# Optimization experiments

Hardware: AMD Instinct MI355X
Metric: run time of the kernel (lower is better)

Reference implementation:

```python
import jax, jax.numpy as jnp
import numpy as np

K = 5            # srn kernel size (kernels[0])
EPSILON = 1e-3   # epsilons -> SRN additive noise scale
BN_EPS = 1e-5
NUM_SLICES = 3
OUT_CH = 64
CLASSES = 5


def _unfold(x, k):
    # torch.nn.Unfold, padding=0: (B, C*k*k, L), channel-major then (kh, kw) row-major
    B, C, H, W = x.shape
    Ho, Wo = H - k + 1, W - k + 1
    cols = jnp.stack([x[:, :, i:i + Ho, j:j + Wo]
                      for i in range(k) for j in range(k)], axis=2)  # (B,C,k*k,Ho,Wo)
    return cols.reshape(B, C * k * k, Ho * Wo), Ho, Wo


def _bn(x, g, b):
    # BatchNorm2d in training mode: batch statistics, biased variance
    m = x.mean((0, 2, 3), keepdims=True)
    v = x.var((0, 2, 3), keepdims=True)
    return (x - m) * jax.lax.rsqrt(v + BN_EPS) * g[None, :, None, None] + b[None, :, None, None]


def _conv(x, w, b):
    y = jax.lax.conv_general_dilated(x, w, (1, 1), 'VALID',
                                     dimension_numbers=('NCHW', 'OIHW', 'NCHW'))
    return y + b[None, :, None, None]


def _avgpool(x, s):
    B, C, H, W = x.shape
    return x.reshape(B, C, H // s, s, W // s, s).mean((3, 5))


def _maxpool(x, s):
    B, C, H, W = x.shape
    return x.reshape(B, C, H // s, s, W // s, s).max((3, 5))


def _srn(x, srn_w):
    B = x.shape[0]
    y, Ho, Wo = _unfold(x, K)                               # (B, n, L)
    y = y + EPSILON * jax.random.normal(jax.random.key(42), y.shape, y.dtype)
    gg = jnp.std(y, axis=1, ddof=1, keepdims=True)          # torch.std is unbiased
    y = y / gg
    O, C, _, _, S = srn_w.shape
    n = C * K * K
    X = srn_w.reshape(O, n, S)
    X = jnp.concatenate([jnp.ones((O, n, 1), X.dtype), X], axis=2)   # (O, n, S+1)
    Xcov = jnp.einsum('onf,ong->ofg', X, X)                 # X^T X, (O, 4, 4)
    Xinv = jnp.linalg.inv(Xcov)
    M = jnp.einsum('ofg,ong->ofn', Xinv, X)
    Wc = jnp.einsum('ofn,bnl->bofl', M, y)
    pred = jnp.einsum('onf,bofl->bonl', X, Wc)              # fitted values (B,O,n,L)
    err = jnp.mean((y[:, None] - pred) ** 2, axis=2)        # (B,O,L)
    err = err.reshape(B, O, Ho, Wo)
    A = (jnp.exp(-err) - np.exp(-1.0)) / (1.0 - np.exp(-1.0))
    return A - 0.5


def setup_inputs() -> dict:
    key = jax.random.key(0)
    ks = jax.random.split(key, 12)
    x = jax.random.normal(ks[0], (4, 3, 64, 64), jnp.float32)
    # xavier-style init scaled up for numerical stability of the small-matrix inverse
    srn_w = 0.05 * jax.random.normal(ks[1], (OUT_CH, 3, K, K, NUM_SLICES), jnp.float32)
    conv2_w = 0.05 * jax.random.normal(ks[2], (128, 64, 3, 3), jnp.float32)
    conv2_b = 0.01 * jax.random.normal(ks[3], (128,), jnp.float32)
    conv3_w = 0.05 * jax.random.normal(ks[4], (128, 128, 3, 3), jnp.float32)
    conv3_b = 0.01 * jax.random.normal(ks[5], (128,), jnp.float32)
    conv4_w = 0.05 * jax.random.normal(ks[6], (128, 128, 3, 3), jnp.float32)
    conv4_b = 0.01 * jax.random.normal(ks[7], (128,), jnp.float32)
    bn1_g = jnp.ones((64,), jnp.float32); bn1_b = jnp.zeros((64,), jnp.float32)
    bn2_g = jnp.ones((128,), jnp.float32); bn2_b = jnp.zeros((128,), jnp.float32)
    bn3_g = jnp.ones((128,), jnp.float32); bn3_b = jnp.zeros((128,), jnp.float32)
    bn4_g = jnp.ones((128,), jnp.float32); bn4_b = jnp.zeros((128,), jnp.float32)
    fc2_w = 0.05 * jax.random.normal(ks[8], (CLASSES, 128, 1, 1), jnp.float32)
    fc2_b = 0.01 * jax.random.normal(ks[9], (CLASSES,), jnp.float32)
    return dict(x=x, srn_w=srn_w, conv2_w=conv2_w, conv2_b=conv2_b,
                conv3_w=conv3_w, conv3_b=conv3_b, conv4_w=conv4_w, conv4_b=conv4_b,
                bn1_g=bn1_g, bn1_b=bn1_b, bn2_g=bn2_g, bn2_b=bn2_b,
                bn3_g=bn3_g, bn3_b=bn3_b, bn4_g=bn4_g, bn4_b=bn4_b,
                fc2_w=fc2_w, fc2_b=fc2_b)


def reference(x, srn_w, conv2_w, conv2_b, conv3_w, conv3_b, conv4_w, conv4_b,
              bn1_g, bn1_b, bn2_g, bn2_b, bn3_g, bn3_b, bn4_g, bn4_b,
              fc2_w, fc2_b):
    h = _srn(x, srn_w)                                      # (B,64,60,60)
    h = _avgpool(h, 2)
    h = _bn(h, bn1_g, bn1_b)
    h = jax.nn.relu(_bn(_conv(h, conv2_w, conv2_b), bn2_g, bn2_b))
    h = _avgpool(h, 2)
    h = jax.nn.relu(_bn(_conv(h, conv3_w, conv3_b), bn3_g, bn3_b))
    h = _maxpool(h, 2)
    h = jax.nn.relu(_bn(_conv(h, conv4_w, conv4_b), bn4_g, bn4_b))
    h = _maxpool(h, 4)                                      # (B,128,1,1)
    flat = h.reshape(h.shape[0], -1)                        # (B,128)
    return flat @ fc2_w.reshape(CLASSES, -1).T + fc2_b      # 1x1 conv == matmul
```

## Files before the change

kernel.cpp:

```cpp
#include <hip/hip_runtime.h>
#include <math.h>

__device__ __align__(16) float g_w2p[9 * 2304 * 4];
__device__ __align__(16) float g_w3p[17 * 2304 * 4];
__device__ __align__(16) float g_w4p[8 * 4608 * 4];
__device__ __align__(16) float g_h1[4 * 30 * 30 * 64];
__device__ __align__(16) float g_h2[4 * 14 * 14 * 4 * 128];
__device__ __align__(16) float g_h3[4 * 6 * 6 * 4 * 128];
__device__ __align__(16) float g_h4[4 * 16 * 128];

__global__ __launch_bounds__(256) void k_srn(const float* __restrict__ x,
                                             const float* __restrict__ srn_w,
                                             const float* __restrict__ w2,
                                             float* __restrict__ stats) {
    __shared__ __align__(16) float wlds[64 * 244];
    __shared__ float xsm[648];
    __shared__ float part[2 * 15 * 66];
    __shared__ float redS[256], redQ[256];
    int bid = blockIdx.x, t = threadIdx.x;
    int b = bid / 60, rem = bid % 60, r = rem >> 1, ch = rem & 1;

    for (int j = bid * 256 + t; j < 73728; j += 240 * 256) {
        int c = j & 3, s4 = j >> 2;
        int sl = s4 % 36, tmp = s4 / 36, oc_l = tmp & 63, blk = tmp >> 6;
        int it = blk & 3, ocg = blk >> 2;
        int kw = sl % 3, icq = (sl / 3) & 3, kh = sl / 12;
        int ic = it * 16 + icq * 4 + c;
        g_w2p[j] = w2[((ocg * 64 + oc_l) * 64 + ic) * 9 + kh * 3 + kw];
    }

    float4 wr[15];
#pragma unroll
    for (int k = 0; k < 15; k++) {
        int i4 = k * 256 + t;
        if (i4 < 3600) wr[k] = ((const float4*)srn_w)[i4];
    }
    float xr[3];
#pragma unroll
    for (int k = 0; k < 3; k++) {
        int i = t + k * 256;
        if (i < 648) {
            int c = i / 216, rm = i % 216, rr = rm / 36, col = rm % 36;
            int gc = ch * 30 + col; if (gc > 63) gc = 63;
            xr[k] = x[((b * 3 + c) * 64 + (2 * r + rr)) * 64 + gc];
        }
    }
#pragma unroll
    for (int k = 0; k < 15; k++) {
        int i4 = k * 256 + t;
        if (i4 < 3600) {
            float v[4] = { wr[k].x, wr[k].y, wr[k].z, wr[k].w };
#pragma unroll
            for (int e = 0; e < 4; e++) {
                int i = i4 * 4 + e, o = i / 225, j = i % 225;
                wlds[o * 244 + (j / 15) * 16 + (j % 15)] = v[e];
            }
        }
    }
#pragma unroll
    for (int k = 0; k < 3; k++) { int i = t + k * 256; if (i < 648) xsm[i] = xr[k]; }
    __syncthreads();

    int w = t >> 6, o = t & 63;
    int rw = w & 1, cq = w >> 1, base = cq * 16;

    float z1[16], z2[16], z3[16], s[16], q[16];
#pragma unroll
    for (int i = 0; i < 16; i++) { z1[i]=0; z2[i]=0; z3[i]=0; s[i]=0; q[i]=0; }

    for (int c = 0; c < 3; c++) {
#pragma unroll
        for (int kh = 0; kh < 5; kh++) {
            float xv[20];
#pragma unroll
            for (int k = 0; k < 20; k++) xv[k] = xsm[(c * 6 + rw + kh) * 36 + base + k];
            float wf[16];
            const float* wp = &wlds[o * 244 + (c * 5 + kh) * 16];
            *(float4*)&wf[0]  = *(const float4*)&wp[0];
            *(float4*)&wf[4]  = *(const float4*)&wp[4];
            *(float4*)&wf[8]  = *(const float4*)&wp[8];
            *(float4*)&wf[12] = *(const float4*)&wp[12];
#pragma unroll
            for (int kw = 0; kw < 5; kw++) {
                float w1 = wf[kw * 3], w2v = wf[kw * 3 + 1], w3v = wf[kw * 3 + 2];
#pragma unroll
                for (int i = 0; i < 16; i++) {
                    float v = xv[kw + i];
                    s[i] += v; q[i] += v * v;
                    z1[i] += w1 * v; z2[i] += w2v * v; z3[i] += w3v * v;
                }
            }
        }
    }

    float gm[16];
    {
        float c01=0,c02=0,c03=0,c11=0,c12=0,c13=0,c22=0,c23=0,c33=0;
#pragma unroll
        for (int row = 0; row < 15; row++) {
            float wf[16];
            const float* wp = &wlds[o * 244 + row * 16];
            *(float4*)&wf[0]  = *(const float4*)&wp[0];
            *(float4*)&wf[4]  = *(const float4*)&wp[4];
            *(float4*)&wf[8]  = *(const float4*)&wp[8];
            *(float4*)&wf[12] = *(const float4*)&wp[12];
#pragma unroll
            for (int kw = 0; kw < 5; kw++) {
                float w1 = wf[kw*3], w2v = wf[kw*3+1], w3v = wf[kw*3+2];
                c01 += w1; c02 += w2v; c03 += w3v;
                c11 += w1*w1; c12 += w1*w2v; c13 += w1*w3v;
                c22 += w2v*w2v; c23 += w2v*w3v; c33 += w3v*w3v;
            }
        }
        float A[4][8];
        A[0][0]=75.f; A[0][1]=c01; A[0][2]=c02; A[0][3]=c03;
        A[1][0]=c01;  A[1][1]=c11; A[1][2]=c12; A[1][3]=c13;
        A[2][0]=c02;  A[2][1]=c12; A[2][2]=c22; A[2][3]=c23;
        A[3][0]=c03;  A[3][1]=c13; A[3][2]=c23; A[3][3]=c33;
#pragma unroll
        for (int i = 0; i < 4; i++)
#pragma unroll
            for (int j = 0; j < 4; j++) A[i][4 + j] = (i == j) ? 1.f : 0.f;
#pragma unroll
        for (int p = 0; p < 4; p++) {
            float ip = 1.f / A[p][p];
#pragma unroll
            for (int j = 0; j < 8; j++) A[p][j] *= ip;
#pragma unroll
            for (int i = 0; i < 4; i++) if (i != p) {
                float f = A[i][p];
#pragma unroll
                for (int j = 0; j < 8; j++) A[i][j] -= f * A[p][j];
            }
        }
#pragma unroll
        for (int i = 0; i < 4; i++)
#pragma unroll
            for (int j = 0; j < 4; j++) gm[i * 4 + j] = A[i][4 + j];
    }

    const float C1 = 0.36787944117144233f;
    const float INV = 1.5819767068693265f;
#pragma unroll
    for (int pp = 0; pp < 8; pp++) {
        int pl = cq * 8 + pp;
        if (pl < 15) {
            float aa = 0.f;
#pragma unroll
            for (int e = 0; e < 2; e++) {
                int i = 2 * pp + e;
                float sum = s[i], sq = q[i];
                float gg2 = (sq - sum * sum * (1.f / 75.f)) * (1.f / 74.f);
                float zf[4] = { sum, z1[i], z2[i], z3[i] };
                float qf = 0.f;
#pragma unroll
                for (int f = 0; f < 4; f++) {
                    float acc = 0.f;
#pragma unroll
                    for (int h = 0; h < 4; h++) acc += gm[f * 4 + h] * zf[h];
                    qf += acc * zf[f];
                }
                float err = (sq - qf) / (75.f * gg2);
                aa += (expf(-err) - C1) * INV - 0.5f;
            }
            part[(rw * 15 + pl) * 66 + o] = 0.25f * aa;
        }
    }
    __syncthreads();

    int j = t >> 6;
    float ps = 0.f, pq = 0.f;
    for (int pl = j; pl < 15; pl += 4) {
        float v = part[pl * 66 + o] + part[(15 + pl) * 66 + o];
        g_h1[((b * 30 + r) * 30 + ch * 15 + pl) * 64 + o] = v;
        ps += v; pq += v * v;
    }
    redS[t] = ps; redQ[t] = pq;
    __syncthreads();
    if (t < 64) {
        atomicAdd(&stats[t],      redS[t] + redS[64 + t] + redS[128 + t] + redS[192 + t]);
        atomicAdd(&stats[64 + t], redQ[t] + redQ[64 + t] + redQ[128 + t] + redQ[192 + t]);
    }
}

__global__ __launch_bounds__(256) void k_conv2(const float* __restrict__ w3,
                                               const float* __restrict__ g1,
                                               const float* __restrict__ b1,
                                               float* __restrict__ stats) {
    __shared__ __align__(16) float ws[64 * 148];
    __shared__ __align__(16) float xs[3 * 30 * 64];
    __shared__ float redS[256], redQ[256];
    int blk = blockIdx.x;
    int b = blk / 56, rem = blk % 56, oh = rem >> 1, ocg = rem & 1;
    int t = threadIdx.x;
    int oc_l = t & 63, qtr = t >> 6, owb = qtr * 7;

    for (int j = blk * 256 + t; j < 147456; j += 224 * 256) {
        int c = j & 3, s4 = j >> 2;
        int sl = s4 % 36, tmp = s4 / 36, oc2 = tmp & 63, bk = tmp >> 6;
        int it = bk & 7, og = bk >> 3;
        int kw = sl % 3, icq = (sl / 3) & 3, kh = sl / 12;
        int ic = it * 16 + icq * 4 + c;
        g_w3p[j] = w3[((og * 64 + oc2) * 128 + ic) * 9 + kh * 3 + kw];
    }

    {
        int icb = (t & 15) * 4;
        float4 S = *(const float4*)&stats[icb], Q = *(const float4*)&stats[64 + icb];
        float4 G4 = *(const float4*)&g1[icb], B4 = *(const float4*)&b1[icb];
        float scv[4], shv[4];
        float mm[4] = { S.x, S.y, S.z, S.w }, qq[4] = { Q.x, Q.y, Q.z, Q.w };
        float gg[4] = { G4.x, G4.y, G4.z, G4.w }, bb[4] = { B4.x, B4.y, B4.z, B4.w };
#pragma unroll
        for (int c = 0; c < 4; c++) {
            float m = mm[c] * (1.f / 3600.f);
            float v = qq[c] * (1.f / 3600.f) - m * m;
            scv[c] = gg[c] * rsqrtf(v + 1e-5f);
            shv[c] = bb[c] - m * scv[c];
        }
        const float4* src4 = (const float4*)(g_h1 + (b * 900 + oh * 30) * 64);
        float4 xr[6];
#pragma unroll
        for (int k = 0; k < 6; k++) { int i4 = t + k * 256; if (i4 < 1440) xr[k] = src4[i4]; }
        const float4* wsrc0 = (const float4*)g_w2p;
        float4 wreg[9];
#pragma unroll
        for (int k = 0; k < 9; k++) wreg[k] = wsrc0[(ocg * 4) * 2304 + k * 256 + t];
#pragma unroll
        for (int k = 0; k < 6; k++) {
            int i4 = t + k * 256;
            if (i4 < 1440) {
                float4 v;
                v.x = xr[k].x * scv[0] + shv[0]; v.y = xr[k].y * scv[1] + shv[1];
                v.z = xr[k].z * scv[2] + shv[2]; v.w = xr[k].w * scv[3] + shv[3];
                *(float4*)&xs[i4 * 4] = v;
            }
        }
#pragma unroll
        for (int k = 0; k < 9; k++) {
            int idx = k * 256 + t;
            *(float4*)&ws[(idx / 36) * 148 + (idx % 36) * 4] = wreg[k];
        }
    }
    __syncthreads();

    float acc[7] = {0, 0, 0, 0, 0, 0, 0};
    const float4* wsrc = (const float4*)g_w2p + (ocg * 4) * 2304;
    for (int it = 0; it < 4; ++it) {
        float4 wreg[9];
        if (it < 3) {
#pragma unroll
            for (int k = 0; k < 9; k++) wreg[k] = wsrc[(it + 1) * 2304 + k * 256 + t];
        }
#pragma unroll 1
        for (int icq = 0; icq < 4; icq++) {
            int xoff = it * 16 + icq * 4;
#pragma unroll
            for (int kh = 0; kh < 3; kh++) {
                const float* wb = &ws[oc_l * 148 + (kh * 4 + icq) * 12];
                float4 w0 = *(const float4*)&wb[0];
                float4 w1 = *(const float4*)&wb[4];
                float4 w2v = *(const float4*)&wb[8];
                const float* xrow = &xs[(kh * 30 + owb) * 64 + xoff];
                float4 x0 = *(const float4*)&xrow[0];
                float4 x1 = *(const float4*)&xrow[64];
#pragma unroll
                for (int i = 0; i < 7; i++) {
                    float4 x2 = *(const float4*)&xrow[(i + 2) * 64];
                    acc[i] += w0.x * x0.x + w0.y * x0.y + w0.z * x0.z + w0.w * x0.w
                            + w1.x * x1.x + w1.y * x1.y + w1.z * x1.z + w1.w * x1.w
                            + w2v.x * x2.x + w2v.y * x2.y + w2v.z * x2.z + w2v.w * x2.w;
                    x0 = x1; x1 = x2;
                }
            }
        }
        if (it < 3) {
            __syncthreads();
#pragma unroll
            for (int k = 0; k < 9; k++) {
                int idx = k * 256 + t;
                *(float4*)&ws[(idx / 36) * 148 + (idx % 36) * 4] = wreg[k];
            }
            __syncthreads();
        }
    }
    int oc = ocg * 64 + oc_l;
    float ps = 0.f, pq = 0.f;
#pragma unroll
    for (int i = 0; i < 7; i++) {
        int ow = owb + i;
        g_h2[(((b * 14 + (oh >> 1)) * 14 + (ow >> 1)) * 4 + (oh & 1) * 2 + (ow & 1)) * 128 + oc] = acc[i];
        ps += acc[i]; pq += acc[i] * acc[i];
    }
    redS[t] = ps; redQ[t] = pq;
    __syncthreads();
    if (t < 64) {
        atomicAdd(&stats[128 + ocg * 64 + t], redS[t] + redS[64 + t] + redS[128 + t] + redS[192 + t]);
        atomicAdd(&stats[256 + ocg * 64 + t], redQ[t] + redQ[64 + t] + redQ[128 + t] + redQ[192 + t]);
    }
}

__global__ __launch_bounds__(256) void k_conv3(const float* __restrict__ w4,
                                               const float* __restrict__ g2,
                                               const float* __restrict__ b2,
                                               float* __restrict__ stats) {
    __shared__ __align__(16) float ws[64 * 148];
    __shared__ __align__(16) float xs[3 * 14 * 128];
    __shared__ float redS[256], redQ[256];
    int blk = blockIdx.x;
    int b = blk / 24, rem = blk % 24, oh = rem >> 1, ocg = rem & 1;
    int t = threadIdx.x;
    int oc_l = t & 63, qtr = t >> 6, owb = qtr * 3;

    for (int j = blk * 256 + t; j < 147456; j += 96 * 256) {
        int c = j & 3, s4 = j >> 2;
        int sl = s4 % 72, tmp = s4 / 72, oc2 = tmp & 15, blkq = tmp >> 4;
        int icq = blkq & 3, og = blkq >> 2;
        int kw = sl % 3, icb2 = (sl / 3) & 7, kh = sl / 24;
        int ic = icq * 32 + icb2 * 4 + c;
        g_w4p[j] = w4[((og * 16 + oc2) * 128 + ic) * 9 + kh * 3 + kw];
    }

    {
        int icb = (t & 31) * 4;
        float4 S = *(const float4*)&stats[128 + icb], Q = *(const float4*)&stats[256 + icb];
        float4 G4 = *(const float4*)&g2[icb], B4 = *(const float4*)&b2[icb];
        float scv[4], shv[4];
        float mm[4] = { S.x, S.y, S.z, S.w }, qq[4] = { Q.x, Q.y, Q.z, Q.w };
        float gg[4] = { G4.x, G4.y, G4.z, G4.w }, bb[4] = { B4.x, B4.y, B4.z, B4.w };
#pragma unroll
        for (int c = 0; c < 4; c++) {
            float m = mm[c] * (1.f / 3136.f);
            float v = qq[c] * (1.f / 3136.f) - m * m;
            scv[c] = gg[c] * rsqrtf(v + 1e-5f);
            shv[c] = bb[c] - m * scv[c];
        }
        const float4* wsrc0 = (const float4*)g_w3p;
        float4 wreg[9];
#pragma unroll
        for (int k = 0; k < 9; k++) wreg[k] = wsrc0[(ocg * 8) * 2304 + k * 256 + t];
        float4 pa[6], pb[6], pc[6], pd[6];
#pragma unroll
        for (int k = 0; k < 6; k++) {
            int i4 = t + k * 256;
            if (i4 < 1344) {
                int px = (i4 >> 5) % 14, rr = i4 / 448;
                const float4* p0 = (const float4*)&g_h2[(((b * 14 + oh + rr) * 14 + px) * 4) * 128 + (i4 & 31) * 4];
                pa[k] = p0[0]; pb[k] = p0[32]; pc[k] = p0[64]; pd[k] = p0[96];
            }
        }
#pragma unroll
        for (int k = 0; k < 9; k++) {
            int idx = k * 256 + t;
            *(float4*)&ws[(idx / 36) * 148 + (idx % 36) * 4] = wreg[k];
        }
#pragma unroll
        for (int k = 0; k < 6; k++) {
            int i4 = t + k * 256;
            if (i4 < 1344) {
                float4 o4;
                o4.x = 0.25f * (fmaxf(pa[k].x * scv[0] + shv[0], 0.f) + fmaxf(pb[k].x * scv[0] + shv[0], 0.f)
                              + fmaxf(pc[k].x * scv[0] + shv[0], 0.f) + fmaxf(pd[k].x * scv[0] + shv[0], 0.f));
                o4.y = 0.25f * (fmaxf(pa[k].y * scv[1] + shv[1], 0.f) + fmaxf(pb[k].y * scv[1] + shv[1], 0.f)
                              + fmaxf(pc[k].y * scv[1] + shv[1], 0.f) + fmaxf(pd[k].y * scv[1] + shv[1], 0.f));
                o4.z = 0.25f * (fmaxf(pa[k].z * scv[2] + shv[2], 0.f) + fmaxf(pb[k].z * scv[2] + shv[2], 0.f)
                              + fmaxf(pc[k].z * scv[2] + shv[2], 0.f) + fmaxf(pd[k].z * scv[2] + shv[2], 0.f));
                o4.w = 0.25f * (fmaxf(pa[k].w * scv[3] + shv[3], 0.f) + fmaxf(pb[k].w * scv[3] + shv[3], 0.f)
                              + fmaxf(pc[k].w * scv[3] + shv[3], 0.f) + fmaxf(pd[k].w * scv[3] + shv[3], 0.f));
                *(float4*)&xs[i4 * 4] = o4;
            }
        }
    }
    __syncthreads();

    float acc[3] = {0, 0, 0};
    const float4* wsrc = (const float4*)g_w3p + (ocg * 8) * 2304;
    for (int it = 0; it < 8; ++it) {
        float4 wreg[9];
        if (it < 7) {
#pragma unroll
            for (int k = 0; k < 9; k++) wreg[k] = wsrc[(it + 1) * 2304 + k * 256 + t];
        }
#pragma unroll 1
        for (int icq = 0; icq < 4; icq++) {
            int xoff = it * 16 + icq * 4;
#pragma unroll
            for (int kh = 0; kh < 3; kh++) {
                const float* wb = &ws[oc_l * 148 + (kh * 4 + icq) * 12];
                float4 w0 = *(const float4*)&wb[0];
                float4 w1 = *(const float4*)&wb[4];
                float4 w2v = *(const float4*)&wb[8];
                const float* xrow = &xs[(kh * 14 + owb) * 128 + xoff];
                float4 x0 = *(const float4*)&xrow[0];
                float4 x1 = *(const float4*)&xrow[128];
#pragma unroll
                for (int i = 0; i < 3; i++) {
                    float4 x2 = *(const float4*)&xrow[(i + 2) * 128];
                    acc[i] += w0.x * x0.x + w0.y * x0.y + w0.z * x0.z + w0.w * x0.w
                            + w1.x * x1.x + w1.y * x1.y + w1.z * x1.z + w1.w * x1.w
                            + w2v.x * x2.x + w2v.y * x2.y + w2v.z * x2.z + w2v.w * x2.w;
                    x0 = x1; x1 = x2;
                }
            }
        }
        if (it < 7) {
            __syncthreads();
#pragma unroll
            for (int k = 0; k < 9; k++) {
                int idx = k * 256 + t;
                *(float4*)&ws[(idx / 36) * 148 + (idx % 36) * 4] = wreg[k];
            }
            __syncthreads();
        }
    }
    int oc = ocg * 64 + oc_l;
    float ps = 0.f, pq = 0.f;
#pragma unroll
    for (int i = 0; i < 3; i++) {
        int ow = owb + i;
        g_h3[(((b * 6 + (oh >> 1)) * 6 + (ow >> 1)) * 4 + (oh & 1) * 2 + (ow & 1)) * 128 + oc] = acc[i];
        ps += acc[i]; pq += acc[i] * acc[i];
    }
    redS[t] = ps; redQ[t] = pq;
    __syncthreads();
    if (t < 64) {
        atomicAdd(&stats[384 + ocg * 64 + t], redS[t] + redS[64 + t] + redS[128 + t] + redS[192 + t]);
        atomicAdd(&stats[512 + ocg * 64 + t], redQ[t] + redQ[64 + t] + redQ[128 + t] + redQ[192 + t]);
    }
}

__global__ __launch_bounds__(256) void k_conv4(const float* __restrict__ g3,
                                               const float* __restrict__ b3,
                                               float* __restrict__ stats) {
    __shared__ __align__(16) float ws[64 * 292];
    __shared__ __align__(16) float xs[3 * 6 * 128];
    __shared__ float red[256];
    int blk = blockIdx.x;
    int b = blk / 32, rem = blk % 32, oh = rem / 8, ocg = rem % 8;
    int t = threadIdx.x;
    int oc_l = t & 15, ow = (t >> 4) & 3, icq = t >> 6;

    {
        int icb = (t & 31) * 4;
        float4 S = *(const float4*)&stats[384 + icb], Q = *(const float4*)&stats[512 + icb];
        float4 G4 = *(const float4*)&g3[icb], B4 = *(const float4*)&b3[icb];
        float scv[4], shv[4];
        float mm[4] = { S.x, S.y, S.z, S.w }, qq[4] = { Q.x, Q.y, Q.z, Q.w };
        float gg[4] = { G4.x, G4.y, G4.z, G4.w }, bb[4] = { B4.x, B4.y, B4.z, B4.w };
#pragma unroll
        for (int c = 0; c < 4; c++) {
            float m = mm[c] * (1.f / 576.f);
            float v = qq[c] * (1.f / 576.f) - m * m;
            scv[c] = gg[c] * rsqrtf(v + 1e-5f);
            shv[c] = bb[c] - m * scv[c];
        }
        const float4* wsrc = (const float4*)g_w4p + ocg * 4608;
        float4 wreg[18];
#pragma unroll
        for (int k = 0; k < 18; k++) wreg[k] = wsrc[k * 256 + t];
        float4 pa[3], pb[3], pc[3], pd[3];
#pragma unroll
        for (int k = 0; k < 3; k++) {
            int i4 = t + k * 256;
            if (i4 < 576) {
                int px = (i4 >> 5) % 6, rr = i4 / 192;
                const float4* p0 = (const float4*)&g_h3[(((b * 6 + oh + rr) * 6 + px) * 4) * 128 + (i4 & 31) * 4];
                pa[k] = p0[0]; pb[k] = p0[32]; pc[k] = p0[64]; pd[k] = p0[96];
            }
        }
#pragma unroll
        for (int k = 0; k < 18; k++) {
            int idx = k * 256 + t;
            *(float4*)&ws[(idx / 72) * 292 + (idx % 72) * 4] = wreg[k];
        }
#pragma unroll
        for (int k = 0; k < 3; k++) {
            int i4 = t + k * 256;
            if (i4 < 576) {
                float4 o4;
                o4.x = fmaxf(fmaxf(fmaxf(pa[k].x * scv[0] + shv[0], pb[k].x * scv[0] + shv[0]),
                                   fmaxf(pc[k].x * scv[0] + shv[0], pd[k].x * scv[0] + shv[0])), 0.f);
                o4.y = fmaxf(fmaxf(fmaxf(pa[k].y * scv[1] + shv[1], pb[k].y * scv[1] + shv[1]),
                                   fmaxf(pc[k].y * scv[1] + shv[1], pd[k].y * scv[1] + shv[1])), 0.f);
                o4.z = fmaxf(fmaxf(fmaxf(pa[k].z * scv[2] + shv[2], pb[k].z * scv[2] + shv[2]),
                                   fmaxf(pc[k].z * scv[2] + shv[2], pd[k].z * scv[2] + shv[2])), 0.f);
                o4.w = fmaxf(fmaxf(fmaxf(pa[k].w * scv[3] + shv[3], pb[k].w * scv[3] + shv[3]),
                                   fmaxf(pc[k].w * scv[3] + shv[3], pd[k].w * scv[3] + shv[3])), 0.f);
                *(float4*)&xs[i4 * 4] = o4;
            }
        }
    }
    __syncthreads();

    float acc = 0.f;
    const float* wbase = &ws[(icq * 16 + oc_l) * 292];
#pragma unroll 1
    for (int icbq = 0; icbq < 8; icbq++) {
#pragma unroll
        for (int kh = 0; kh < 3; kh++) {
            const float* wb = &wbase[(kh * 8 + icbq) * 12];
            float4 w0 = *(const float4*)&wb[0];
            float4 w1 = *(const float4*)&wb[4];
            float4 w2v = *(const float4*)&wb[8];
            float4 x0 = *(const float4*)&xs[(kh * 6 + ow) * 128 + icq * 32 + icbq * 4];
            float4 x1 = *(const float4*)&xs[(kh * 6 + ow + 1) * 128 + icq * 32 + icbq * 4];
            float4 x2 = *(const float4*)&xs[(kh * 6 + ow + 2) * 128 + icq * 32 + icbq * 4];
            acc += w0.x * x0.x + w0.y * x0.y + w0.z * x0.z + w0.w * x0.w
                 + w1.x * x1.x + w1.y * x1.y + w1.z * x1.z + w1.w * x1.w
                 + w2v.x * x2.x + w2v.y * x2.y + w2v.z * x2.z + w2v.w * x2.w;
        }
    }
    red[t] = acc;
    __syncthreads();
    if (t < 64) {
        float v = red[t] + red[t + 64] + red[t + 128] + red[t + 192];
        int oc = ocg * 16 + (t & 15);
        g_h4[((b * 4 + oh) * 4 + (t >> 4)) * 128 + oc] = v;
        float ps = v + __shfl_xor(v, 16);  ps += __shfl_xor(ps, 32);
        float pv = v * v;
        float pq = pv + __shfl_xor(pv, 16); pq += __shfl_xor(pq, 32);
        if (t < 16) {
            atomicAdd(&stats[640 + ocg * 16 + t], ps);
            atomicAdd(&stats[768 + ocg * 16 + t], pq);
        }
    }
}

__global__ __launch_bounds__(256) void k_final(const float* __restrict__ g4,
                                               const float* __restrict__ b4,
                                               const float* __restrict__ fcw,
                                               const float* __restrict__ fcb,
                                               const float* __restrict__ stats,
                                               float* __restrict__ out) {
    __shared__ float sc[128], sh[128];
    __shared__ float pooled[4][128];
    int t = threadIdx.x;
    if (t < 128) {
        float m = stats[640 + t] * (1.f / 64.f);
        float v = stats[768 + t] * (1.f / 64.f) - m * m;
        float rs = rsqrtf(v + 1e-5f);
        sc[t] = g4[t] * rs; sh[t] = b4[t] - m * sc[t];
    }
    __syncthreads();
    for (int item = t; item < 512; item += 256) {
        int b = item >> 7, oc = item & 127;
        float s = sc[oc], h = sh[oc];
        float mx = 0.f;
#pragma unroll
        for (int k = 0; k < 16; k++) mx = fmaxf(mx, g_h4[(b * 16 + k) * 128 + oc] * s + h);
        pooled[b][oc] = mx;
    }
    __syncthreads();
    if (t < 20) {
        int b = t / 5, cls = t % 5;
        float acc = fcb[cls];
        const float* w = &fcw[cls * 128];
        for (int oc = 0; oc < 128; oc++) acc += pooled[b][oc] * w[oc];
        out[b * 5 + cls] = acc;
    }
}

extern "C" void kernel_launch(void* const* d_in, const int* in_sizes, int n_in,
                              void* d_out, int out_size, void* d_ws, size_t ws_size,
                              hipStream_t stream) {
    (void)in_sizes; (void)n_in; (void)out_size; (void)ws_size;
    const float* x     = (const float*)d_in[0];
    const float* srn_w = (const float*)d_in[1];
    const float* w2    = (const float*)d_in[2];
    const float* w3    = (const float*)d_in[4];
    const float* w4    = (const float*)d_in[6];
    const float* g1 = (const float*)d_in[8];  const float* b1 = (const float*)d_in[9];
    const float* g2 = (const float*)d_in[10]; const float* b2 = (const float*)d_in[11];
    const float* g3 = (const float*)d_in[12]; const float* b3 = (const float*)d_in[13];
    const float* g4 = (const float*)d_in[14]; const float* b4 = (const float*)d_in[15];
    const float* fcw = (const float*)d_in[16]; const float* fcb = (const float*)d_in[17];
    float* out = (float*)d_out;
    float* stats = (float*)d_ws;

    hipMemsetAsync(d_ws, 0, 4096, stream);
    k_srn  <<<dim3(240), dim3(256), 0, stream>>>(x, srn_w, w2, stats);
    k_conv2<<<dim3(224), dim3(256), 0, stream>>>(w3, g1, b1, stats);
    k_conv3<<<dim3(96),  dim3(256), 0, stream>>>(w4, g2, b2, stats);
    k_conv4<<<dim3(128), dim3(256), 0, stream>>>(g3, b3, stats);
    k_final<<<dim3(1),   dim3(256), 0, stream>>>(g4, b4, fcw, fcb, stats, out);
}
```

Measured before the change: 111.2 us.

## Split conv2 and conv3 output width across two blocks to double grid size

Conv2 and conv3 now split each output row's width into two halves, each handled by its own block. This doubles the grids to 448 and 192 blocks so more of the GPU's compute units are busy. Each block stages a smaller input tile and computes fewer outputs per thread, with uneven per-wave work (4/4/3/3 and 2/2/1/1). The trade-off is that each block still loads a full weight slice, so weight traffic per output doubles and the loops gain divergent guards.

```diff
diff --git a/kernel.cpp b/kernel.cpp
--- a/kernel.cpp
+++ b/kernel.cpp
@@ -49,11 +49,11 @@
     for (int k = 0; k < 15; k++) {
         int i4 = k * 256 + t;
         if (i4 < 3600) {
-            float v[4] = { wr[k].x, wr[k].y, wr[k].z, wr[k].w };
+            float v4[4] = { wr[k].x, wr[k].y, wr[k].z, wr[k].w };
 #pragma unroll
             for (int e = 0; e < 4; e++) {
-                int i = i4 * 4 + e, o = i / 225, j = i % 225;
-                wlds[o * 244 + (j / 15) * 16 + (j % 15)] = v[e];
+                int i = i4 * 4 + e, o = i / 225, jj = i % 225;
+                wlds[o * 244 + (jj / 15) * 16 + (jj % 15)] = v4[e];
             }
         }
     }
@@ -168,9 +168,9 @@
     }
     __syncthreads();
 
-    int j = t >> 6;
+    int j2 = t >> 6;
     float ps = 0.f, pq = 0.f;
-    for (int pl = j; pl < 15; pl += 4) {
+    for (int pl = j2; pl < 15; pl += 4) {
         float v = part[pl * 66 + o] + part[(15 + pl) * 66 + o];
         g_h1[((b * 30 + r) * 30 + ch * 15 + pl) * 64 + o] = v;
         ps += v; pq += v * v;
@@ -188,14 +188,16 @@
                                                const float* __restrict__ b1,
                                                float* __restrict__ stats) {
     __shared__ __align__(16) float ws[64 * 148];
-    __shared__ __align__(16) float xs[3 * 30 * 64];
+    __shared__ __align__(16) float xs[3 * 16 * 64];
     __shared__ float redS[256], redQ[256];
-    int blk = blockIdx.x;
-    int b = blk / 56, rem = blk % 56, oh = rem >> 1, ocg = rem & 1;
-    int t = threadIdx.x;
-    int oc_l = t & 63, qtr = t >> 6, owb = qtr * 7;
-
-    for (int j = blk * 256 + t; j < 147456; j += 224 * 256) {
+    int blk = blockIdx.x, t = threadIdx.x;
+    int b = blk / 112, rem = blk % 112, oh = rem >> 2, sub = rem & 3;
+    int owh = sub >> 1, ocg = sub & 1;
+    int oc_l = t & 63, qtr = t >> 6;
+    int now = (qtr < 2) ? 4 : 3;
+    int lowb = (qtr < 2) ? qtr * 4 : 8 + (qtr - 2) * 3;
+
+    for (int j = blk * 256 + t; j < 147456; j += 448 * 256) {
         int c = j & 3, s4 = j >> 2;
         int sl = s4 % 36, tmp = s4 / 36, oc2 = tmp & 63, bk = tmp >> 6;
         int it = bk & 7, og = bk >> 3;
@@ -218,23 +220,21 @@
             scv[c] = gg[c] * rsqrtf(v + 1e-5f);
             shv[c] = bb[c] - m * scv[c];
         }
-        const float4* src4 = (const float4*)(g_h1 + (b * 900 + oh * 30) * 64);
-        float4 xr[6];
-#pragma unroll
-        for (int k = 0; k < 6; k++) { int i4 = t + k * 256; if (i4 < 1440) xr[k] = src4[i4]; }
+        int px = t >> 4, ic4 = t & 15;
+        float4 xr[3];
+#pragma unroll
+        for (int k = 0; k < 3; k++)
+            xr[k] = ((const float4*)g_h1)[((b * 30 + oh + k) * 30 + owh * 14 + px) * 16 + ic4];
         const float4* wsrc0 = (const float4*)g_w2p;
         float4 wreg[9];
 #pragma unroll
         for (int k = 0; k < 9; k++) wreg[k] = wsrc0[(ocg * 4) * 2304 + k * 256 + t];
 #pragma unroll
-        for (int k = 0; k < 6; k++) {
-            int i4 = t + k * 256;
-            if (i4 < 1440) {
-                float4 v;
-                v.x = xr[k].x * scv[0] + shv[0]; v.y = xr[k].y * scv[1] + shv[1];
-                v.z = xr[k].z * scv[2] + shv[2]; v.w = xr[k].w * scv[3] + shv[3];
-                *(float4*)&xs[i4 * 4] = v;
-            }
+        for (int k = 0; k < 3; k++) {
+            float4 v;
+            v.x = xr[k].x * scv[0] + shv[0]; v.y = xr[k].y * scv[1] + shv[1];
+            v.z = xr[k].z * scv[2] + shv[2]; v.w = xr[k].w * scv[3] + shv[3];
+            *(float4*)&xs[((k * 16 + px) * 16 + ic4) * 4] = v;
         }
 #pragma unroll
         for (int k = 0; k < 9; k++) {
@@ -244,7 +244,7 @@
     }
     __syncthreads();
 
-    float acc[7] = {0, 0, 0, 0, 0, 0, 0};
+    float acc[4] = {0, 0, 0, 0};
     const float4* wsrc = (const float4*)g_w2p + (ocg * 4) * 2304;
     for (int it = 0; it < 4; ++it) {
         float4 wreg[9];
@@ -261,16 +261,18 @@
                 float4 w0 = *(const float4*)&wb[0];
                 float4 w1 = *(const float4*)&wb[4];
                 float4 w2v = *(const float4*)&wb[8];
-                const float* xrow = &xs[(kh * 30 + owb) * 64 + xoff];
+                const float* xrow = &xs[(kh * 16 + lowb) * 64 + xoff];
                 float4 x0 = *(const float4*)&xrow[0];
                 float4 x1 = *(const float4*)&xrow[64];
 #pragma unroll
-                for (int i = 0; i < 7; i++) {
-                    float4 x2 = *(const float4*)&xrow[(i + 2) * 64];
-                    acc[i] += w0.x * x0.x + w0.y * x0.y + w0.z * x0.z + w0.w * x0.w
-                            + w1.x * x1.x + w1.y * x1.y + w1.z * x1.z + w1.w * x1.w
-                            + w2v.x * x2.x + w2v.y * x2.y + w2v.z * x2.z + w2v.w * x2.w;
-                    x0 = x1; x1 = x2;
+                for (int i = 0; i < 4; i++) {
+                    if (i < now) {
+                        float4 x2 = *(const float4*)&xrow[(i + 2) * 64];
+                        acc[i] += w0.x * x0.x + w0.y * x0.y + w0.z * x0.z + w0.w * x0.w
+                                + w1.x * x1.x + w1.y * x1.y + w1.z * x1.z + w1.w * x1.w
+                                + w2v.x * x2.x + w2v.y * x2.y + w2v.z * x2.z + w2v.w * x2.w;
+                        x0 = x1; x1 = x2;
+                    }
                 }
             }
         }
@@ -287,10 +289,12 @@
     int oc = ocg * 64 + oc_l;
     float ps = 0.f, pq = 0.f;
 #pragma unroll
-    for (int i = 0; i < 7; i++) {
-        int ow = owb + i;
-        g_h2[(((b * 14 + (oh >> 1)) * 14 + (ow >> 1)) * 4 + (oh & 1) * 2 + (ow & 1)) * 128 + oc] = acc[i];
-        ps += acc[i]; pq += acc[i] * acc[i];
+    for (int i = 0; i < 4; i++) {
+        if (i < now) {
+            int ow = owh * 14 + lowb + i;
+            g_h2[(((b * 14 + (oh >> 1)) * 14 + (ow >> 1)) * 4 + (oh & 1) * 2 + (ow & 1)) * 128 + oc] = acc[i];
+            ps += acc[i]; pq += acc[i] * acc[i];
+        }
     }
     redS[t] = ps; redQ[t] = pq;
     __syncthreads();
@@ -305,14 +309,16 @@
                                                const float* __restrict__ b2,
                                                float* __restrict__ stats) {
     __shared__ __align__(16) float ws[64 * 148];
-    __shared__ __align__(16) float xs[3 * 14 * 128];
+    __shared__ __align__(16) float xs[3 * 8 * 128];
     __shared__ float redS[256], redQ[256];
-    int blk = blockIdx.x;
-    int b = blk / 24, rem = blk % 24, oh = rem >> 1, ocg = rem & 1;
-    int t = threadIdx.x;
-    int oc_l = t & 63, qtr = t >> 6, owb = qtr * 3;
-
-    for (int j = blk * 256 + t; j < 147456; j += 96 * 256) {
+    int blk = blockIdx.x, t = threadIdx.x;
+    int b = blk / 48, rem = blk % 48, oh = rem >> 2, sub = rem & 3;
+    int owh = sub >> 1, ocg = sub & 1;
+    int oc_l = t & 63, qtr = t >> 6;
+    int now = (qtr < 2) ? 2 : 1;
+    int lowb = (qtr < 2) ? qtr * 2 : 4 + (qtr - 2);
+
+    for (int j = blk * 256 + t; j < 147456; j += 192 * 256) {
         int c = j & 3, s4 = j >> 2;
         int sl = s4 % 72, tmp = s4 / 72, oc2 = tmp & 15, blkq = tmp >> 4;
         int icq = blkq & 3, og = blkq >> 2;
@@ -339,15 +345,12 @@
         float4 wreg[9];
 #pragma unroll
         for (int k = 0; k < 9; k++) wreg[k] = wsrc0[(ocg * 8) * 2304 + k * 256 + t];
-        float4 pa[6], pb[6], pc[6], pd[6];
-#pragma unroll
-        for (int k = 0; k < 6; k++) {
-            int i4 = t + k * 256;
-            if (i4 < 1344) {
-                int px = (i4 >> 5) % 14, rr = i4 / 448;
-                const float4* p0 = (const float4*)&g_h2[(((b * 14 + oh + rr) * 14 + px) * 4) * 128 + (i4 & 31) * 4];
-                pa[k] = p0[0]; pb[k] = p0[32]; pc[k] = p0[64]; pd[k] = p0[96];
-            }
+        int px = (t >> 5) & 7, ic4 = t & 31;
+        float4 pa[3], pb[3], pc[3], pd[3];
+#pragma unroll
+        for (int k = 0; k < 3; k++) {
+            const float4* p0 = (const float4*)&g_h2[(((b * 14 + oh + k) * 14 + owh * 6 + px) * 4) * 128 + ic4 * 4];
+            pa[k] = p0[0]; pb[k] = p0[32]; pc[k] = p0[64]; pd[k] = p0[96];
         }
 #pragma unroll
         for (int k = 0; k < 9; k++) {
@@ -355,25 +358,22 @@
             *(float4*)&ws[(idx / 36) * 148 + (idx % 36) * 4] = wreg[k];
         }
 #pragma unroll
-        for (int k = 0; k < 6; k++) {
-            int i4 = t + k * 256;
-            if (i4 < 1344) {
-                float4 o4;
-                o4.x = 0.25f * (fmaxf(pa[k].x * scv[0] + shv[0], 0.f) + fmaxf(pb[k].x * scv[0] + shv[0], 0.f)
-                              + fmaxf(pc[k].x * scv[0] + shv[0], 0.f) + fmaxf(pd[k].x * scv[0] + shv[0], 0.f));
-                o4.y = 0.25f * (fmaxf(pa[k].y * scv[1] + shv[1], 0.f) + fmaxf(pb[k].y * scv[1] + shv[1], 0.f)
-                              + fmaxf(pc[k].y * scv[1] + shv[1], 0.f) + fmaxf(pd[k].y * scv[1] + shv[1], 0.f));
-                o4.z = 0.25f * (fmaxf(pa[k].z * scv[2] + shv[2], 0.f) + fmaxf(pb[k].z * scv[2] + shv[2], 0.f)
-                              + fmaxf(pc[k].z * scv[2] + shv[2], 0.f) + fmaxf(pd[k].z * scv[2] + shv[2], 0.f));
-                o4.w = 0.25f * (fmaxf(pa[k].w * scv[3] + shv[3], 0.f) + fmaxf(pb[k].w * scv[3] + shv[3], 0.f)
-                              + fmaxf(pc[k].w * scv[3] + shv[3], 0.f) + fmaxf(pd[k].w * scv[3] + shv[3], 0.f));
-                *(float4*)&xs[i4 * 4] = o4;
-            }
-        }
-    }
-    __syncthreads();
-
-    float acc[3] = {0, 0, 0};
+        for (int k = 0; k < 3; k++) {
+            float4 o4;
+            o4.x = 0.25f * (fmaxf(pa[k].x * scv[0] + shv[0], 0.f) + fmaxf(pb[k].x * scv[0] + shv[0], 0.f)
+                          + fmaxf(pc[k].x * scv[0] + shv[0], 0.f) + fmaxf(pd[k].x * scv[0] + shv[0], 0.f));
+            o4.y = 0.25f * (fmaxf(pa[k].y * scv[1] + shv[1], 0.f) + fmaxf(pb[k].y * scv[1] + shv[1], 0.f)
+                          + fmaxf(pc[k].y * scv[1] + shv[1], 0.f) + fmaxf(pd[k].y * scv[1] + shv[1], 0.f));
+            o4.z = 0.25f * (fmaxf(pa[k].z * scv[2] + shv[2], 0.f) + fmaxf(pb[k].z * scv[2] + shv[2], 0.f)
+                          + fmaxf(pc[k].z * scv[2] + shv[2], 0.f) + fmaxf(pd[k].z * scv[2] + shv[2], 0.f));
+            o4.w = 0.25f * (fmaxf(pa[k].w * scv[3] + shv[3], 0.f) + fmaxf(pb[k].w * scv[3] + shv[3], 0.f)
+                          + fmaxf(pc[k].w * scv[3] + shv[3], 0.f) + fmaxf(pd[k].w * scv[3] + shv[3], 0.f));
+            *(float4*)&xs[((k * 8 + px) * 32 + ic4) * 4] = o4;
+        }
+    }
+    __syncthreads();
+
+    float acc[2] = {0, 0};
     const float4* wsrc = (const float4*)g_w3p + (ocg * 8) * 2304;
     for (int it = 0; it < 8; ++it) {
         float4 wreg[9];
@@ -390,16 +390,18 @@
                 float4 w0 = *(const float4*)&wb[0];
                 float4 w1 = *(const float4*)&wb[4];
                 float4 w2v = *(const float4*)&wb[8];
-                const float* xrow = &xs[(kh * 14 + owb) * 128 + xoff];
+                const float* xrow = &xs[(kh * 8 + lowb) * 128 + xoff];
                 float4 x0 = *(const float4*)&xrow[0];
                 float4 x1 = *(const float4*)&xrow[128];
 #pragma unroll
-                for (int i = 0; i < 3; i++) {
-                    float4 x2 = *(const float4*)&xrow[(i + 2) * 128];
-                    acc[i] += w0.x * x0.x + w0.y * x0.y + w0.z * x0.z + w0.w * x0.w
-                            + w1.x * x1.x + w1.y * x1.y + w1.z * x1.z + w1.w * x1.w
-                            + w2v.x * x2.x + w2v.y * x2.y + w2v.z * x2.z + w2v.w * x2.w;
-                    x0 = x1; x1 = x2;
+                for (int i = 0; i < 2; i++) {
+                    if (i < now) {
+                        float4 x2 = *(const float4*)&xrow[(i + 2) * 128];
+                        acc[i] += w0.x * x0.x + w0.y * x0.y + w0.z * x0.z + w0.w * x0.w
+                                + w1.x * x1.x + w1.y * x1.y + w1.z * x1.z + w1.w * x1.w
+                                + w2v.x * x2.x + w2v.y * x2.y + w2v.z * x2.z + w2v.w * x2.w;
+                        x0 = x1; x1 = x2;
+                    }
                 }
             }
         }
@@ -416,10 +418,12 @@
     int oc = ocg * 64 + oc_l;
     float ps = 0.f, pq = 0.f;
 #pragma unroll
-    for (int i = 0; i < 3; i++) {
-        int ow = owb + i;
-        g_h3[(((b * 6 + (oh >> 1)) * 6 + (ow >> 1)) * 4 + (oh & 1) * 2 + (ow & 1)) * 128 + oc] = acc[i];
-        ps += acc[i]; pq += acc[i] * acc[i];
+    for (int i = 0; i < 2; i++) {
+        if (i < now) {
+            int ow = owh * 6 + lowb + i;
+            g_h3[(((b * 6 + (oh >> 1)) * 6 + (ow >> 1)) * 4 + (oh & 1) * 2 + (ow & 1)) * 128 + oc] = acc[i];
+            ps += acc[i]; pq += acc[i] * acc[i];
+        }
     }
     redS[t] = ps; redQ[t] = pq;
     __syncthreads();
@@ -435,9 +439,8 @@
     __shared__ __align__(16) float ws[64 * 292];
     __shared__ __align__(16) float xs[3 * 6 * 128];
     __shared__ float red[256];
-    int blk = blockIdx.x;
+    int blk = blockIdx.x, t = threadIdx.x;
     int b = blk / 32, rem = blk % 32, oh = rem / 8, ocg = rem % 8;
-    int t = threadIdx.x;
     int oc_l = t & 15, ow = (t >> 4) & 3, icq = t >> 6;
 
     {
@@ -543,20 +546,20 @@
     }
     __syncthreads();
     for (int item = t; item < 512; item += 256) {
-        int b = item >> 7, oc = item & 127;
+        int bb = item >> 7, oc = item & 127;
         float s = sc[oc], h = sh[oc];
         float mx = 0.f;
 #pragma unroll
-        for (int k = 0; k < 16; k++) mx = fmaxf(mx, g_h4[(b * 16 + k) * 128 + oc] * s + h);
-        pooled[b][oc] = mx;
+        for (int k = 0; k < 16; k++) mx = fmaxf(mx, g_h4[(bb * 16 + k) * 128 + oc] * s + h);
+        pooled[bb][oc] = mx;
     }
     __syncthreads();
     if (t < 20) {
-        int b = t / 5, cls = t % 5;
+        int bb = t / 5, cls = t % 5;
         float acc = fcb[cls];
         const float* w = &fcw[cls * 128];
-        for (int oc = 0; oc < 128; oc++) acc += pooled[b][oc] * w[oc];
-        out[b * 5 + cls] = acc;
+        for (int oc = 0; oc < 128; oc++) acc += pooled[bb][oc] * w[oc];
+        out[bb * 5 + cls] = acc;
     }
 }
 
@@ -579,8 +582,8 @@
 
     hipMemsetAsync(d_ws, 0, 4096, stream);
     k_srn  <<<dim3(240), dim3(256), 0, stream>>>(x, srn_w, w2, stats);
-    k_conv2<<<dim3(224), dim3(256), 0, stream>>>(w3, g1, b1, stats);
-    k_conv3<<<dim3(96),  dim3(256), 0, stream>>>(w4, g2, b2, stats);
+    k_conv2<<<dim3(448), dim3(256), 0, stream>>>(w3, g1, b1, stats);
+    k_conv3<<<dim3(192), dim3(256), 0, stream>>>(w4, g2, b2, stats);
     k_conv4<<<dim3(128), dim3(256), 0, stream>>>(g3, b3, stats);
     k_final<<<dim3(1),   dim3(256), 0, stream>>>(g4, b4, fcw, fcb, stats, out);
 }
```

Measured after the change: 113.7 us. 1.02x slower.
